# Kernel tuning notes

Measured on AMD Instinct MI355X. Metric: run time of the kernel, lower is better.

Reference implementation:

```python
import jax, jax.numpy as jnp
import numpy as np

N, E, G = 50000, 800000, 64
IN, HID, T, EDGE_DIM, HLS = 32, 64, 2, 2, 32
# deg histogram: all nodes degree 16 -> avg_deg['log'] = log(16+1)
AVG_LOG = float(np.log(17.0))


def _pna(x, src, dst, eattr, We, be, Wpre, bpre, Wpost, bpost, Wlin, blin):
    """PNAConv with aggregators [mean,min,max,std], scalers [identity,amp,att],
    towers=T, pre_layers=1, post_layers=1, divide_input=False."""
    n, F = x.shape
    enc = eattr @ We + be                                   # [E, F] edge encoder
    # message: concat(x_i, x_j, edge) -> per-tower Linear(3F -> F)
    h = jnp.concatenate([x[dst], x[src], enc], axis=-1)     # [E, 3F] (same for all towers)
    m = jnp.einsum('ef,tfo->eto', h, Wpre) + bpre           # [E, T, F]
    ones = jnp.ones((m.shape[0],), m.dtype)
    cnt = jax.ops.segment_sum(ones, dst, num_segments=n)    # in-degree [N]
    d = jnp.maximum(cnt, 1.0)[:, None, None]
    s = jax.ops.segment_sum(m, dst, num_segments=n)
    mean = s / d
    msq = jax.ops.segment_sum(m * m, dst, num_segments=n) / d
    std = jnp.sqrt(jax.nn.relu(msq - mean * mean) + 1e-5)
    has = (cnt > 0)[:, None, None]
    mn = jnp.where(has, jax.ops.segment_min(m, dst, num_segments=n), 0.0)
    mx = jnp.where(has, jax.ops.segment_max(m, dst, num_segments=n), 0.0)
    agg = jnp.concatenate([mean, mn, mx, std], axis=-1)     # [N, T, 4F]
    logd = jnp.log(d + 1.0)
    scaled = jnp.concatenate([agg, agg * (logd / AVG_LOG), agg * (AVG_LOG / logd)], axis=-1)  # [N,T,12F]
    xt = jnp.broadcast_to(x[:, None, :], (n, Wpre.shape[0], F))
    out = jnp.concatenate([xt, scaled], axis=-1)            # [N, T, 13F]
    o = jnp.einsum('nti,tio->nto', out, Wpost) + bpost      # [N, T, F_out]
    return o.reshape(n, -1) @ Wlin + blin                   # [N, HID]


def setup_inputs():
    key = jax.random.key(0)
    ks = iter(jax.random.split(key, 48))
    def p(shape):
        return jax.random.normal(next(ks), shape, jnp.float32) * 0.05
    inp = {}
    inp['x'] = jax.random.normal(next(ks), (N, IN), jnp.float32)
    inp['edge_attr'] = jax.random.normal(next(ks), (E, EDGE_DIM), jnp.float32)
    inp['hls_attr'] = jax.random.normal(next(ks), (G, HLS), jnp.float32)
    inp['edge_index'] = jax.random.randint(next(ks), (2, E), 0, N)
    inp['batch'] = jnp.sort(jax.random.randint(next(ks), (N,), 0, G))
    Fo = HID // T
    for l, Fin in enumerate([IN, HID]):
        inp[f'We{l}'] = p((EDGE_DIM, Fin)); inp[f'be{l}'] = jnp.zeros((Fin,), jnp.float32)
        inp[f'Wpre{l}'] = p((T, 3 * Fin, Fin)); inp[f'bpre{l}'] = jnp.zeros((T, Fin), jnp.float32)
        inp[f'Wpost{l}'] = p((T, 13 * Fin, Fo)); inp[f'bpost{l}'] = jnp.zeros((T, Fo), jnp.float32)
        inp[f'Wlin{l}'] = p((HID, HID)); inp[f'blin{l}'] = jnp.zeros((HID,), jnp.float32)
    inp['W1'] = p((HID + HLS, 64)); inp['b1'] = jnp.zeros((64,), jnp.float32)
    inp['W2'] = p((64, 64)); inp['b2'] = jnp.zeros((64,), jnp.float32)
    inp['W3'] = p((64, 1)); inp['b3'] = jnp.zeros((1,), jnp.float32)
    return inp


def reference(x, edge_attr, hls_attr,
              We0, be0, Wpre0, bpre0, Wpost0, bpost0, Wlin0, blin0,
              We1, be1, Wpre1, bpre1, Wpost1, bpost1, Wlin1, blin1,
              W1, b1, W2, b2, W3, b3,
              edge_index, batch):
    src, dst = edge_index[0], edge_index[1]
    h = jax.nn.relu(_pna(x, src, dst, edge_attr, We0, be0, Wpre0, bpre0, Wpost0, bpost0, Wlin0, blin0))
    h = jax.nn.relu(_pna(h, src, dst, edge_attr, We1, be1, Wpre1, bpre1, Wpost1, bpost1, Wlin1, blin1))
    g = jax.ops.segment_sum(h, batch, num_segments=G)       # global_add_pool [G, HID]
    g = jnp.concatenate([g, hls_attr], axis=-1)
    g = jax.nn.relu(g @ W1 + b1)
    g = jax.nn.relu(g @ W2 + b2)
    return g @ W3 + b3                                      # [G, 1]
```

## Files before the change

### kernel.cpp

```cpp
#include <hip/hip_runtime.h>
#include <math.h>
#include <float.h>

#define NN 50000
#define EE 800000
#define CAP 64

#define NB 196
#define SPAN 256
#define BCAP 4608

typedef unsigned short ushort_t;
typedef short short8 __attribute__((ext_vector_type(8)));
typedef float floatx4 __attribute__((ext_vector_type(4)));

__device__ __constant__ float kAVG_LOG = 2.8332133440562162f;

__device__ inline ushort_t f2bf(float v) {
    union { float f; unsigned u; } x; x.f = v;
    unsigned r = x.u + 0x7fffu + ((x.u >> 16) & 1u);
    return (ushort_t)(r >> 16);
}
__device__ inline float bf2f(ushort_t b) {
    union { unsigned u; float f; } x; x.u = ((unsigned)b) << 16; return x.f;
}
__device__ inline float bitsf(unsigned u) {
    union { unsigned u; float f; } x; x.u = u; return x.f;
}
__device__ inline void splitbf(float v, ushort_t& hi, ushort_t& lo) {
    hi = f2bf(v);
    lo = f2bf(v - bf2f(hi));
}

template <int F>
__device__ void prep_ab_dev(const float* __restrict__ We, const float* __restrict__ be,
                            const float* __restrict__ Wpre, const float* __restrict__ bpre,
                            float* __restrict__ U, float* __restrict__ Wab,
                            float* __restrict__ bias_ab) {
    const int TF = 2 * F;
    int tid = threadIdx.x;
    for (int idx = tid; idx < 2 * TF; idx += 256) {
        int c = idx / TF, f = idx % TF;
        int t = f / F, o = f % F;
        float s = 0.f;
        for (int g = 0; g < F; ++g)
            s += We[c * F + g] * Wpre[((size_t)t * 3 * F + 2 * F + g) * F + o];
        U[idx] = s;
    }
    for (int idx = tid; idx < F * 2 * TF; idx += 256) {
        int g = idx / (2 * TF), cc = idx % (2 * TF);
        int t, o, row;
        if (cc < TF) { t = cc / F; o = cc % F; row = g; }
        else { int c2 = cc - TF; t = c2 / F; o = c2 % F; row = F + g; }
        Wab[idx] = Wpre[((size_t)t * 3 * F + row) * F + o];
    }
    for (int cc = tid; cc < 2 * TF; cc += 256) {
        float v = 0.f;
        if (cc < TF) {
            int t = cc / F, o = cc % F;
            float s = 0.f;
            for (int g = 0; g < F; ++g)
                s += be[g] * Wpre[((size_t)t * 3 * F + 2 * F + g) * F + o];
            v = s + bpre[t * F + o];
        }
        bias_ab[cc] = v;
    }
}

template <int F>
__device__ void prep_zf_elem(int idx, const float* __restrict__ Wpost, const float* __restrict__ Wlin,
                             ushort_t* __restrict__ Bh, ushort_t* __restrict__ Bl) {
    const int KT = 9 * F;
    int jg = idx / KT, k = idx - jg * KT;
    int b = jg >> 6, j = jg & 63;
    float v = 0.f;
    if (k < F) {
        if (b == 0) {
#pragma unroll
            for (int t = 0; t < 2; ++t)
#pragma unroll
                for (int c = 0; c < 32; ++c)
                    v += Wpost[((size_t)t * 13 * F + k) * 32 + c] * Wlin[(t * 32 + c) * 64 + j];
        }
    } else {
        int r = k - F;
        int t = r / (4 * F), rr = r - t * 4 * F;
#pragma unroll
        for (int c = 0; c < 32; ++c)
            v += Wpost[((size_t)t * 13 * F + F + b * 4 * F + rr) * 32 + c] * Wlin[(t * 32 + c) * 64 + j];
    }
    ushort_t h_, l_;
    splitbf(v, h_, l_);
    Bh[(size_t)jg * KT + k] = h_;
    Bl[(size_t)jg * KT + k] = l_;
}

#define NZ0 216
#define NZ1 432
#define PREPB (NZ0 + NZ1 + 3)
#define INITB 6250

__global__ __launch_bounds__(256) void prep_init(
    const float* We0, const float* be0, const float* Wpre0, const float* bpre0,
    const float* Wpost0, const float* Wlin0, const float* bpost0, const float* blin0,
    const float* We1, const float* be1, const float* Wpre1, const float* bpre1,
    const float* Wpost1, const float* Wlin1, const float* bpost1, const float* blin1,
    float* U0, float* Wab0, float* bias_ab0, ushort_t* Bh0, ushort_t* Bl0, float* bias_zf0,
    float* U1, float* Wab1, float* bias_ab1, ushort_t* Bh1, ushort_t* Bl1, float* bias_zf1,
    int* gcount, float* pool, const float* __restrict__ x, ushort_t* __restrict__ xb) {
    int b = blockIdx.x;
    int tid = threadIdx.x;
    if (b >= PREPB) {
        int i = (b - PREPB) * 256 + tid;
        if (i < NN * 32) xb[i] = f2bf(x[i]);
        if (i < NB) gcount[i] = 0;
        if (i < 64 * 64) pool[i] = 0.f;
        return;
    }
    if (b < NZ0) {
        prep_zf_elem<32>(b * 256 + tid, Wpost0, Wlin0, Bh0, Bl0);
    } else if (b < NZ0 + NZ1) {
        prep_zf_elem<64>((b - NZ0) * 256 + tid, Wpost1, Wlin1, Bh1, Bl1);
    } else if (b == NZ0 + NZ1) {
        prep_ab_dev<32>(We0, be0, Wpre0, bpre0, U0, Wab0, bias_ab0);
    } else if (b == NZ0 + NZ1 + 1) {
        prep_ab_dev<64>(We1, be1, Wpre1, bpre1, U1, Wab1, bias_ab1);
    } else {
        for (int j = tid; j < 64; j += 256) {
            float s0 = blin0[j], s1 = blin1[j];
#pragma unroll
            for (int t = 0; t < 2; ++t)
#pragma unroll
                for (int c = 0; c < 32; ++c) {
                    s0 += bpost0[t * 32 + c] * Wlin0[(t * 32 + c) * 64 + j];
                    s1 += bpost1[t * 32 + c] * Wlin1[(t * 32 + c) * 64 + j];
                }
            bias_zf0[j] = s0;
            bias_zf1[j] = s1;
        }
    }
}

__global__ __launch_bounds__(1024) void partition_edges(
    const int* __restrict__ ei, const float* __restrict__ ea,
    int* __restrict__ gcount, uint2* __restrict__ part) {
    __shared__ int hist[NB];
    __shared__ int lbase[NB];
    int tid = threadIdx.x;
    int e0 = blockIdx.x * 4096;
    for (int i = tid; i < NB; i += 1024) hist[i] = 0;
    __syncthreads();
    int bq[4], rnk[4];
    unsigned px[4], py[4];
#pragma unroll
    for (int q = 0; q < 4; ++q) {
        int e = e0 + q * 1024 + tid;
        bq[q] = -1;
        if (e < EE) {
            int s = ei[e];
            int d = ei[EE + e];
            float2 v = *(const float2*)(ea + 2 * e);
            bq[q] = d >> 8;
            px[q] = ((unsigned)(d & 255) << 16) | (unsigned)s;
            py[q] = ((unsigned)f2bf(v.y) << 16) | (unsigned)f2bf(v.x);
            rnk[q] = atomicAdd(&hist[bq[q]], 1);
        }
    }
    __syncthreads();
    for (int i = tid; i < NB; i += 1024)
        lbase[i] = atomicAdd(&gcount[i], hist[i]);
    __syncthreads();
#pragma unroll
    for (int q = 0; q < 4; ++q) {
        if (bq[q] >= 0) {
            int slot = lbase[bq[q]] + rnk[q];
            if (slot < BCAP)
                part[(size_t)bq[q] * BCAP + slot] = make_uint2(px[q], py[q]);
        }
    }
}

__device__ void csr_fill_block(int g, const int* __restrict__ gcount,
                               const uint2* __restrict__ part,
                               int* __restrict__ cnt, uint2* __restrict__ csr) {
    __shared__ int lcnt[SPAN];
    int tid = threadIdx.x;
    lcnt[tid] = 0;
    __syncthreads();
    int total = gcount[g];
    if (total > BCAP) total = BCAP;
    size_t pbase = (size_t)g * BCAP;
    for (int i = tid; i < total; i += 256) {
        uint2 rec = part[pbase + i];
        int rel = rec.x >> 16;
        int src = rec.x & 0xffff;
        int p = atomicAdd(&lcnt[rel], 1);
        if (p < CAP) {
            int node = (g << 8) + rel;
            csr[(size_t)node * CAP + p] = make_uint2((unsigned)src, rec.y);
        }
    }
    __syncthreads();
    int node = (g << 8) + tid;
    if (node < NN) cnt[node] = lcnt[tid];
}

__device__ void gemm_bias_block(const float* __restrict__ A, const float* __restrict__ B,
                                const float* __restrict__ bias, float* __restrict__ Ca,
                                ushort_t* __restrict__ Cb, int M, int K, int Ncols, int bstart,
                                int mb, int cb) {
    __shared__ float As[32][132];
    __shared__ float Bs[32][68];
    int m0 = mb * 128, c0 = cb * 64;
    int tid = threadIdx.x;
    int tx = tid & 15, ty = tid >> 4;
    int ms = tid >> 3, u = tid & 7;
    float acc[8][4] = {};
    for (int k0 = 0; k0 < K; k0 += 32) {
#pragma unroll
        for (int p = 0; p < 4; ++p) {
            int m = ms + 32 * p;
            int gm = m0 + m;
            float4 v = make_float4(0.f, 0.f, 0.f, 0.f);
            if (gm < M) v = *(const float4*)(A + (size_t)gm * K + k0 + u * 4);
            As[u * 4 + 0][m] = v.x; As[u * 4 + 1][m] = v.y;
            As[u * 4 + 2][m] = v.z; As[u * 4 + 3][m] = v.w;
        }
#pragma unroll
        for (int p = 0; p < 2; ++p) {
            int idx = tid + 256 * p;
            int kk = idx >> 4, q = idx & 15;
            *(float4*)&Bs[kk][q * 4] = *(const float4*)(B + (size_t)(k0 + kk) * Ncols + c0 + q * 4);
        }
        __syncthreads();
#pragma unroll 8
        for (int k = 0; k < 32; ++k) {
            float a0[8], b0[4];
            *(float4*)&a0[0] = *(const float4*)&As[k][ty * 8];
            *(float4*)&a0[4] = *(const float4*)&As[k][ty * 8 + 4];
            *(float4*)&b0[0] = *(const float4*)&Bs[k][tx * 4];
#pragma unroll
            for (int i = 0; i < 8; ++i)
#pragma unroll
                for (int j = 0; j < 4; ++j) acc[i][j] = fmaf(a0[i], b0[j], acc[i][j]);
        }
        __syncthreads();
    }
    float bj[4];
#pragma unroll
    for (int j = 0; j < 4; ++j) bj[j] = bias[c0 + tx * 4 + j];
    bool bside = (c0 >= bstart);
    int TFw = bstart;
#pragma unroll
    for (int i = 0; i < 8; ++i) {
        int gm = m0 + ty * 8 + i;
        if (gm >= M) continue;
        float v0 = acc[i][0] + bj[0], v1 = acc[i][1] + bj[1];
        float v2 = acc[i][2] + bj[2], v3 = acc[i][3] + bj[3];
        if (!bside) {
            *(float4*)(Ca + (size_t)gm * TFw + c0 + tx * 4) = make_float4(v0, v1, v2, v3);
        } else {
            ushort4 w;
            w.x = f2bf(v0); w.y = f2bf(v1); w.z = f2bf(v2); w.w = f2bf(v3);
            *(ushort4*)(Cb + (size_t)gm * TFw + (c0 - bstart) + tx * 4) = w;
        }
    }
}

__global__ __launch_bounds__(256) void gemm_bias(const float* __restrict__ A, const float* __restrict__ B,
                                                 const float* __restrict__ bias, float* __restrict__ Ca,
                                                 ushort_t* __restrict__ Cb, int M, int K, int Ncols, int bstart) {
    gemm_bias_block(A, B, bias, Ca, Cb, M, K, Ncols, bstart, blockIdx.x, blockIdx.y);
}

__global__ __launch_bounds__(256) void csr_gemm0(
    const int* __restrict__ gcount, const uint2* __restrict__ part,
    int* __restrict__ cnt, uint2* __restrict__ csr,
    const float* __restrict__ A, const float* __restrict__ B, const float* __restrict__ bias,
    float* __restrict__ Ca, ushort_t* __restrict__ Cb) {
    int bx = blockIdx.x;
    if (bx % 5 == 0) {
        csr_fill_block(bx / 5, gcount, part, cnt, csr);
    } else {
        int idx = bx - 1 - bx / 5;
        gemm_bias_block(A, B, bias, Ca, Cb, NN, 32, 128, 64, idx % 391, idx / 391);
    }
}

template <int F>
__global__ __launch_bounds__(256) void aggregate(const float* __restrict__ ABa, const ushort_t* __restrict__ ABb,
                                                 const int* __restrict__ cnt, const uint2* __restrict__ csr,
                                                 const float* __restrict__ U,
                                                 ushort_t* __restrict__ agg_b, float2* __restrict__ sc) {
    const int TF = 2 * F;
    const int FPL = TF / 64;
    int lane = threadIdx.x & 63;
    int n = blockIdx.x * 4 + (threadIdx.x >> 6);
    if (n >= NN) return;
    n = __builtin_amdgcn_readfirstlane(n);
    int f0 = FPL * lane;

    float base[FPL], u0[FPL], u1[FPL], sum[FPL], sq[FPL], mn[FPL], mx[FPL];
#pragma unroll
    for (int r = 0; r < FPL; ++r) {
        base[r] = ABa[(size_t)n * TF + f0 + r];
        u0[r] = U[f0 + r];
        u1[r] = U[TF + f0 + r];
        sum[r] = 0.f; sq[r] = 0.f; mn[r] = FLT_MAX; mx[r] = -FLT_MAX;
    }
    int deg = cnt[n];
    int ec = deg < CAP ? deg : CAP;
    const uint2* __restrict__ p = csr + (size_t)n * CAP;

    int e = 0;
    for (; e + 8 <= ec; e += 8) {
        uint4 c0 = *(const uint4*)(p + e);
        uint4 c1 = *(const uint4*)(p + e + 2);
        uint4 c2 = *(const uint4*)(p + e + 4);
        uint4 c3 = *(const uint4*)(p + e + 6);
        unsigned sb[8] = {c0.x, c0.z, c1.x, c1.z, c2.x, c2.z, c3.x, c3.z};
        unsigned ep[8] = {c0.y, c0.w, c1.y, c1.w, c2.y, c2.w, c3.y, c3.w};
        unsigned wv[8];
#pragma unroll
        for (int i = 0; i < 8; ++i) {
            const ushort_t* row = ABb + (size_t)sb[i] * TF;
            if constexpr (FPL == 2)
                wv[i] = *(const unsigned*)(row + f0);
            else
                wv[i] = row[f0];
        }
#pragma unroll
        for (int i = 0; i < 8; ++i) {
            float ex = bitsf(ep[i] << 16);
            float ey = bitsf(ep[i] & 0xffff0000u);
            float v[FPL];
            if constexpr (FPL == 2) {
                v[0] = bitsf(wv[i] << 16);
                v[1] = bitsf(wv[i] & 0xffff0000u);
            } else {
                v[0] = bitsf(wv[i] << 16);
            }
#pragma unroll
            for (int r = 0; r < FPL; ++r) {
                float q = fmaf(ex, u0[r], fmaf(ey, u1[r], v[r]));
                sum[r] += q;
                sq[r] = fmaf(q, q, sq[r]);
                mn[r] = fminf(mn[r], q);
                mx[r] = fmaxf(mx[r], q);
            }
        }
    }
    for (; e < ec; ++e) {
        uint2 ent = p[e];
        const ushort_t* row = ABb + (size_t)ent.x * TF;
        unsigned wvt;
        if constexpr (FPL == 2) wvt = *(const unsigned*)(row + f0);
        else wvt = row[f0];
        float ex = bitsf(ent.y << 16);
        float ey = bitsf(ent.y & 0xffff0000u);
        float v[FPL];
        if constexpr (FPL == 2) {
            v[0] = bitsf(wvt << 16);
            v[1] = bitsf(wvt & 0xffff0000u);
        } else {
            v[0] = bitsf(wvt << 16);
        }
#pragma unroll
        for (int r = 0; r < FPL; ++r) {
            float q = fmaf(ex, u0[r], fmaf(ey, u1[r], v[r]));
            sum[r] += q;
            sq[r] = fmaf(q, q, sq[r]);
            mn[r] = fminf(mn[r], q);
            mx[r] = fmaxf(mx[r], q);
        }
    }

    float d = (float)(deg > 1 ? deg : 1);
    float inv_d = 1.f / d;
    bool has = deg > 0;
#pragma unroll
    for (int r = 0; r < FPL; ++r) {
        float mean_q = sum[r] * inv_d;
        float var = sq[r] * inv_d - mean_q * mean_q;
        float stdv = sqrtf(fmaxf(var, 0.f) + 1e-5f);
        float mean = has ? base[r] + mean_q : 0.f;
        float vmn = has ? base[r] + mn[r] : 0.f;
        float vmx = has ? base[r] + mx[r] : 0.f;
        int f = f0 + r;
        int t = f / F, o = f - t * F;
        size_t rowb = (size_t)n * (4 * TF) + (size_t)t * (4 * F);
        agg_b[rowb + o] = f2bf(mean);
        agg_b[rowb + F + o] = f2bf(vmn);
        agg_b[rowb + 2 * F + o] = f2bf(vmx);
        agg_b[rowb + 3 * F + o] = f2bf(stdv);
    }
    if (lane == 0) {
        float logd = logf(d + 1.f);
        sc[n] = make_float2(logd / kAVG_LOG, kAVG_LOG / logd);
    }
}

template <int F, bool POOL>
__global__ __launch_bounds__(256, 4) void gemm_zf(
    const ushort_t* __restrict__ xs_b, const ushort_t* __restrict__ agg_b,
    const ushort_t* __restrict__ Bh, const ushort_t* __restrict__ Bl,
    const float* __restrict__ bias_zf, const float2* __restrict__ sc,
    float* __restrict__ H, ushort_t* __restrict__ H_b,
    const int* __restrict__ batch, float* __restrict__ pool) {
    const int KT = 9 * F;
    extern __shared__ char smem[];
    ushort_t* A_s  = (ushort_t*)smem;
    ushort_t* Bh_s = A_s + 64 * 40;
    ushort_t* Bl_s = Bh_s + 192 * 40;
    float* hbuf = (float*)smem;

    int m0 = blockIdx.x * 64;
    int tid = threadIdx.x;
    int lane = tid & 63;
    int wave = tid >> 6;
    int ln = lane & 15, quad = lane >> 4;

    floatx4 acc[4][3];
#pragma unroll
    for (int i = 0; i < 4; ++i)
#pragma unroll
        for (int j = 0; j < 3; ++j) acc[i][j] = (floatx4)(0.f);

    int arow = tid >> 2, asg = tid & 3;
    int bcol[3], bsg[3];
#pragma unroll
    for (int p = 0; p < 3; ++p) {
        int idx = tid + 256 * p;
        bcol[p] = idx >> 2;
        bsg[p] = idx & 3;
    }

    const short8 zero8 = {0, 0, 0, 0, 0, 0, 0, 0};
    short8 pa, pbh[3], pbl[3];
    {
        int c0 = asg * 8;
        int gm = m0 + arow;
        pa = zero8;
        if (gm < NN) pa = *(const short8*)(xs_b + (size_t)gm * F + c0);
#pragma unroll
        for (int p = 0; p < 3; ++p) {
            pbh[p] = *(const short8*)(Bh + (size_t)bcol[p] * KT + bsg[p] * 8);
            pbl[p] = *(const short8*)(Bl + (size_t)bcol[p] * KT + bsg[p] * 8);
        }
    }

    for (int k0 = 0; k0 < KT; k0 += 32) {
        *(short8*)&A_s[arow * 40 + asg * 8] = pa;
#pragma unroll
        for (int p = 0; p < 3; ++p) {
            *(short8*)&Bh_s[bcol[p] * 40 + bsg[p] * 8] = pbh[p];
            *(short8*)&Bl_s[bcol[p] * 40 + bsg[p] * 8] = pbl[p];
        }
        __syncthreads();
        short8 bh[3], bl[3];
#pragma unroll
        for (int b = 0; b < 3; ++b) {
            int col = b * 64 + wave * 16 + ln;
            bh[b] = *(short8*)&Bh_s[col * 40 + quad * 8];
            bl[b] = *(short8*)&Bl_s[col * 40 + quad * 8];
        }
        int kn = k0 + 32;
        if (kn < KT) {
            int c0 = kn + asg * 8;
            int gm = m0 + arow;
            pa = zero8;
            if (gm < NN) {
                pa = (c0 < F) ? *(const short8*)(xs_b + (size_t)gm * F + c0)
                              : *(const short8*)(agg_b + (size_t)gm * 8 * F + (c0 - F));
            }
#pragma unroll
            for (int p = 0; p < 3; ++p) {
                pbh[p] = *(const short8*)(Bh + (size_t)bcol[p] * KT + kn + bsg[p] * 8);
                pbl[p] = *(const short8*)(Bl + (size_t)bcol[p] * KT + kn + bsg[p] * 8);
            }
        }
#pragma unroll
        for (int rf = 0; rf < 4; ++rf) {
            short8 ah = *(short8*)&A_s[(rf * 16 + ln) * 40 + quad * 8];
#pragma unroll
            for (int b = 0; b < 3; ++b) {
                acc[rf][b] = __builtin_amdgcn_mfma_f32_16x16x32_bf16(ah, bh[b], acc[rf][b], 0, 0, 0);
                acc[rf][b] = __builtin_amdgcn_mfma_f32_16x16x32_bf16(ah, bl[b], acc[rf][b], 0, 0, 0);
            }
        }
        __syncthreads();
    }

    int ocol = wave * 16 + ln;
    float bcolv = bias_zf[ocol];

#pragma unroll
    for (int rf = 0; rf < 4; ++rf) {
#pragma unroll
        for (int reg = 0; reg < 4; ++reg) {
            int r = rf * 16 + quad * 4 + reg;
            int gm = m0 + r;
            float2 s = make_float2(0.f, 0.f);
            if (gm < NN) s = sc[gm];
            float y = acc[rf][0][reg] + s.x * acc[rf][1][reg] + s.y * acc[rf][2][reg] + bcolv;
            y = fmaxf(y, 0.f);
            if (POOL) {
                hbuf[r * 68 + ocol] = (gm < NN) ? y : 0.f;
            } else if (gm < NN) {
                H[(size_t)gm * 64 + ocol] = y;
                H_b[(size_t)gm * 64 + ocol] = f2bf(y);
            }
        }
    }
    if (POOL) {
        __syncthreads();
        int col = tid & 63, grp = tid >> 6;
        float a = 0.f;
        int cur = -1;
        for (int i = 0; i < 16; ++i) {
            int r = grp * 16 + i;
            int gm = m0 + r;
            if (gm >= NN) break;
            int b = batch[gm];
            if (b != cur) {
                if (cur >= 0) atomicAdd(&pool[cur * 64 + col], a);
                cur = b; a = 0.f;
            }
            a += hbuf[r * 68 + col];
        }
        if (cur >= 0) atomicAdd(&pool[cur * 64 + col], a);
    }
}

__global__ __launch_bounds__(256) void head_kernel(const float* __restrict__ gpool, const float* __restrict__ hls,
                                                   const float* __restrict__ W1, const float* __restrict__ b1,
                                                   const float* __restrict__ W2, const float* __restrict__ b2,
                                                   const float* __restrict__ W3, const float* __restrict__ b3,
                                                   float* __restrict__ out) {
    __shared__ float gin[64][96];
    __shared__ float r1[64][64];
    __shared__ float r2[64][64];
    int tid = threadIdx.x;
    for (int idx = tid; idx < 64 * 96; idx += 256) {
        int g = idx / 96, j = idx % 96;
        gin[g][j] = (j < 64) ? gpool[g * 64 + j] : hls[g * 32 + (j - 64)];
    }
    __syncthreads();
    for (int idx = tid; idx < 64 * 64; idx += 256) {
        int g = idx / 64, j = idx % 64;
        float acc = b1[j];
        for (int k = 0; k < 96; ++k) acc = fmaf(gin[g][k], W1[k * 64 + j], acc);
        r1[g][j] = fmaxf(acc, 0.f);
    }
    __syncthreads();
    for (int idx = tid; idx < 64 * 64; idx += 256) {
        int g = idx / 64, j = idx % 64;
        float acc = b2[j];
        for (int k = 0; k < 64; ++k) acc = fmaf(r1[g][k], W2[k * 64 + j], acc);
        r2[g][j] = fmaxf(acc, 0.f);
    }
    __syncthreads();
    if (tid < 64) {
        float acc = b3[0];
        for (int k = 0; k < 64; ++k) acc = fmaf(r2[tid][k], W3[k], acc);
        out[tid] = acc;
    }
}

extern "C" void kernel_launch(void* const* d_in, const int* in_sizes, int n_in,
                              void* d_out, int out_size, void* d_ws, size_t ws_size,
                              hipStream_t stream) {
    (void)in_sizes; (void)n_in; (void)out_size; (void)ws_size;
    const float* x     = (const float*)d_in[0];
    const float* eattr = (const float*)d_in[1];
    const float* hls   = (const float*)d_in[2];
    const int*   eidx  = (const int*)d_in[3];
    const int*   batch = (const int*)d_in[4];
    const float* We[2]    = {(const float*)d_in[5],  (const float*)d_in[13]};
    const float* be[2]    = {(const float*)d_in[6],  (const float*)d_in[14]};
    const float* Wpre[2]  = {(const float*)d_in[7],  (const float*)d_in[15]};
    const float* bpre[2]  = {(const float*)d_in[8],  (const float*)d_in[16]};
    const float* Wpost[2] = {(const float*)d_in[9],  (const float*)d_in[17]};
    const float* bpost[2] = {(const float*)d_in[10], (const float*)d_in[18]};
    const float* Wlin[2]  = {(const float*)d_in[11], (const float*)d_in[19]};
    const float* blin[2]  = {(const float*)d_in[12], (const float*)d_in[20]};
    const float* W1 = (const float*)d_in[21]; const float* b1 = (const float*)d_in[22];
    const float* W2 = (const float*)d_in[23]; const float* b2 = (const float*)d_in[24];
    const float* W3 = (const float*)d_in[25]; const float* b3 = (const float*)d_in[26];
    float* out = (float*)d_out;

    char* ws = (char*)d_ws;
    size_t off = 0;
    auto carve = [&](size_t bytes) -> char* {
        char* p = ws + off;
        off = (off + bytes + 255) & ~(size_t)255;
        return p;
    };
    int*      cnt      = (int*)carve((size_t)NN * 4);
    uint2*    csr      = (uint2*)carve((size_t)NN * CAP * 8);
    float*    ABa      = (float*)carve((size_t)NN * 128 * 4);
    ushort_t* ABb      = (ushort_t*)carve((size_t)NN * 128 * 2);
    ushort_t* agg_b    = (ushort_t*)carve((size_t)NN * 512 * 2);
    float2*   sc       = (float2*)carve((size_t)NN * 8);
    ushort_t* xs_b     = (ushort_t*)carve((size_t)NN * 32 * 2);
    float*    h1       = (float*)carve((size_t)NN * 64 * 4);
    ushort_t* h1_b     = (ushort_t*)carve((size_t)NN * 64 * 2);
    float*    U0       = (float*)carve(256 * 4);
    float*    U1       = (float*)carve(256 * 4);
    float*    Wab0     = (float*)carve(16384 * 4);
    float*    Wab1     = (float*)carve(16384 * 4);
    float*    bias_ab0 = (float*)carve(256 * 4);
    float*    bias_ab1 = (float*)carve(256 * 4);
    ushort_t* Bh0      = (ushort_t*)carve((size_t)192 * 288 * 2);
    ushort_t* Bl0      = (ushort_t*)carve((size_t)192 * 288 * 2);
    ushort_t* Bh1      = (ushort_t*)carve((size_t)192 * 576 * 2);
    ushort_t* Bl1      = (ushort_t*)carve((size_t)192 * 576 * 2);
    float*    bias_zf0 = (float*)carve(64 * 4);
    float*    bias_zf1 = (float*)carve(64 * 4);
    float*    pool     = (float*)carve(64 * 64 * 4);
    int*      gcount   = (int*)carve(NB * 4);
    uint2*    part     = (uint2*)agg_b;

    const int MB128 = (NN + 127) / 128;
    const int MB64  = (NN + 63) / 64;
    const int SMEM_ZF = (64 * 40 + 192 * 40 + 192 * 40) * 2;
    const int FUSEDB = NB + MB128 * 2;

    prep_init<<<PREPB + INITB, 256, 0, stream>>>(
        We[0], be[0], Wpre[0], bpre[0], Wpost[0], Wlin[0], bpost[0], blin[0],
        We[1], be[1], Wpre[1], bpre[1], Wpost[1], Wlin[1], bpost[1], blin[1],
        U0, Wab0, bias_ab0, Bh0, Bl0, bias_zf0,
        U1, Wab1, bias_ab1, Bh1, Bl1, bias_zf1,
        gcount, pool, x, xs_b);

    partition_edges<<<(EE + 4095) / 4096, 1024, 0, stream>>>(eidx, eattr, gcount, part);

    csr_gemm0<<<FUSEDB, 256, 0, stream>>>(gcount, part, cnt, csr, x, Wab0, bias_ab0, ABa, ABb);
    aggregate<32><<<(NN + 3) / 4, 256, 0, stream>>>(ABa, ABb, cnt, csr, U0, agg_b, sc);
    gemm_zf<32, false><<<MB64, 256, SMEM_ZF, stream>>>(xs_b, agg_b, Bh0, Bl0, bias_zf0, sc,
                                                       h1, h1_b, batch, pool);

    gemm_bias<<<dim3(MB128, 4), 256, 0, stream>>>(h1, Wab1, bias_ab1, ABa, ABb, NN, 64, 256, 128);
    aggregate<64><<<(NN + 3) / 4, 256, 0, stream>>>(ABa, ABb, cnt, csr, U1, agg_b, sc);
    gemm_zf<64, true><<<MB64, 256, SMEM_ZF, stream>>>(h1_b, agg_b, Bh1, Bl1, bias_zf1, sc,
                                                      nullptr, nullptr, batch, pool);

    head_kernel<<<1, 256, 0, stream>>>(pool, hls, W1, b1, W2, b2, W3, b3, out);
}
```

Before: 349.9 us.

## Enlarge gemm_zf tile to 128 rows, load A directly, double-buffer B

The gemm_zf kernel now covers 128 rows per block instead of 64. Each wave loads its A fragments straight from global memory into registers, skipping the shared-memory A staging. The B tiles are double-buffered in shared memory, which drops one __syncthreads per k-step. This cuts barrier and LDS traffic and reuses each B tile across more rows, at the cost of more registers (8x3 accumulators plus 8 A fragments), occupancy lowered to 2 blocks per SIMD, and redundant A loads across the four waves.

```diff
diff --git a/kernel.cpp b/kernel.cpp
--- a/kernel.cpp
+++ b/kernel.cpp
@@ -401,32 +401,31 @@
 }
 
 template <int F, bool POOL>
-__global__ __launch_bounds__(256, 4) void gemm_zf(
+__global__ __launch_bounds__(256, 2) void gemm_zf(
     const ushort_t* __restrict__ xs_b, const ushort_t* __restrict__ agg_b,
     const ushort_t* __restrict__ Bh, const ushort_t* __restrict__ Bl,
     const float* __restrict__ bias_zf, const float2* __restrict__ sc,
     float* __restrict__ H, ushort_t* __restrict__ H_b,
     const int* __restrict__ batch, float* __restrict__ pool) {
     const int KT = 9 * F;
+    const int SEG = 192 * 40;
     extern __shared__ char smem[];
-    ushort_t* A_s  = (ushort_t*)smem;
-    ushort_t* Bh_s = A_s + 64 * 40;
-    ushort_t* Bl_s = Bh_s + 192 * 40;
+    ushort_t* Bh_s = (ushort_t*)smem;
+    ushort_t* Bl_s = Bh_s + 2 * SEG;
     float* hbuf = (float*)smem;
 
-    int m0 = blockIdx.x * 64;
+    int m0 = blockIdx.x * 128;
     int tid = threadIdx.x;
     int lane = tid & 63;
     int wave = tid >> 6;
     int ln = lane & 15, quad = lane >> 4;
 
-    floatx4 acc[4][3];
-#pragma unroll
-    for (int i = 0; i < 4; ++i)
+    floatx4 acc[8][3];
+#pragma unroll
+    for (int i = 0; i < 8; ++i)
 #pragma unroll
         for (int j = 0; j < 3; ++j) acc[i][j] = (floatx4)(0.f);
 
-    int arow = tid >> 2, asg = tid & 3;
     int bcol[3], bsg[3];
 #pragma unroll
     for (int p = 0; p < 3; ++p) {
@@ -436,43 +435,41 @@
     }
 
     const short8 zero8 = {0, 0, 0, 0, 0, 0, 0, 0};
-    short8 pa, pbh[3], pbl[3];
-    {
-        int c0 = asg * 8;
-        int gm = m0 + arow;
-        pa = zero8;
-        if (gm < NN) pa = *(const short8*)(xs_b + (size_t)gm * F + c0);
+    short8 pbh[3], pbl[3];
+#pragma unroll
+    for (int p = 0; p < 3; ++p) {
+        pbh[p] = *(const short8*)(Bh + (size_t)bcol[p] * KT + bsg[p] * 8);
+        pbl[p] = *(const short8*)(Bl + (size_t)bcol[p] * KT + bsg[p] * 8);
+    }
+
+    int cur = 0;
+    for (int k0 = 0; k0 < KT; k0 += 32) {
 #pragma unroll
         for (int p = 0; p < 3; ++p) {
-            pbh[p] = *(const short8*)(Bh + (size_t)bcol[p] * KT + bsg[p] * 8);
-            pbl[p] = *(const short8*)(Bl + (size_t)bcol[p] * KT + bsg[p] * 8);
-        }
-    }
-
-    for (int k0 = 0; k0 < KT; k0 += 32) {
-        *(short8*)&A_s[arow * 40 + asg * 8] = pa;
-#pragma unroll
-        for (int p = 0; p < 3; ++p) {
-            *(short8*)&Bh_s[bcol[p] * 40 + bsg[p] * 8] = pbh[p];
-            *(short8*)&Bl_s[bcol[p] * 40 + bsg[p] * 8] = pbl[p];
+            *(short8*)&Bh_s[cur * SEG + bcol[p] * 40 + bsg[p] * 8] = pbh[p];
+            *(short8*)&Bl_s[cur * SEG + bcol[p] * 40 + bsg[p] * 8] = pbl[p];
+        }
+        short8 ah[8];
+        int c0 = k0 + quad * 8;
+#pragma unroll
+        for (int rf = 0; rf < 8; ++rf) {
+            int gm = m0 + rf * 16 + ln;
+            ah[rf] = zero8;
+            if (gm < NN) {
+                ah[rf] = (c0 < F) ? *(const short8*)(xs_b + (size_t)gm * F + c0)
+                                  : *(const short8*)(agg_b + (size_t)gm * 8 * F + (c0 - F));
+            }
         }
         __syncthreads();
         short8 bh[3], bl[3];
 #pragma unroll
         for (int b = 0; b < 3; ++b) {
             int col = b * 64 + wave * 16 + ln;
-            bh[b] = *(short8*)&Bh_s[col * 40 + quad * 8];
-            bl[b] = *(short8*)&Bl_s[col * 40 + quad * 8];
+            bh[b] = *(short8*)&Bh_s[cur * SEG + col * 40 + quad * 8];
+            bl[b] = *(short8*)&Bl_s[cur * SEG + col * 40 + quad * 8];
         }
         int kn = k0 + 32;
         if (kn < KT) {
-            int c0 = kn + asg * 8;
-            int gm = m0 + arow;
-            pa = zero8;
-            if (gm < NN) {
-                pa = (c0 < F) ? *(const short8*)(xs_b + (size_t)gm * F + c0)
-                              : *(const short8*)(agg_b + (size_t)gm * 8 * F + (c0 - F));
-            }
 #pragma unroll
             for (int p = 0; p < 3; ++p) {
                 pbh[p] = *(const short8*)(Bh + (size_t)bcol[p] * KT + kn + bsg[p] * 8);
@@ -480,22 +477,23 @@
             }
         }
 #pragma unroll
-        for (int rf = 0; rf < 4; ++rf) {
-            short8 ah = *(short8*)&A_s[(rf * 16 + ln) * 40 + quad * 8];
+        for (int rf = 0; rf < 8; ++rf) {
 #pragma unroll
             for (int b = 0; b < 3; ++b) {
-                acc[rf][b] = __builtin_amdgcn_mfma_f32_16x16x32_bf16(ah, bh[b], acc[rf][b], 0, 0, 0);
-                acc[rf][b] = __builtin_amdgcn_mfma_f32_16x16x32_bf16(ah, bl[b], acc[rf][b], 0, 0, 0);
+                acc[rf][b] = __builtin_amdgcn_mfma_f32_16x16x32_bf16(ah[rf], bh[b], acc[rf][b], 0, 0, 0);
+                acc[rf][b] = __builtin_amdgcn_mfma_f32_16x16x32_bf16(ah[rf], bl[b], acc[rf][b], 0, 0, 0);
             }
         }
-        __syncthreads();
+        cur ^= 1;
     }
 
     int ocol = wave * 16 + ln;
     float bcolv = bias_zf[ocol];
 
-#pragma unroll
-    for (int rf = 0; rf < 4; ++rf) {
+    if (POOL) __syncthreads();
+
+#pragma unroll
+    for (int rf = 0; rf < 8; ++rf) {
 #pragma unroll
         for (int reg = 0; reg < 4; ++reg) {
             int r = rf * 16 + quad * 4 + reg;
@@ -516,19 +514,19 @@
         __syncthreads();
         int col = tid & 63, grp = tid >> 6;
         float a = 0.f;
-        int cur = -1;
-        for (int i = 0; i < 16; ++i) {
-            int r = grp * 16 + i;
+        int cur2 = -1;
+        for (int i = 0; i < 32; ++i) {
+            int r = grp * 32 + i;
             int gm = m0 + r;
             if (gm >= NN) break;
             int b = batch[gm];
-            if (b != cur) {
-                if (cur >= 0) atomicAdd(&pool[cur * 64 + col], a);
-                cur = b; a = 0.f;
+            if (b != cur2) {
+                if (cur2 >= 0) atomicAdd(&pool[cur2 * 64 + col], a);
+                cur2 = b; a = 0.f;
             }
             a += hbuf[r * 68 + col];
         }
-        if (cur >= 0) atomicAdd(&pool[cur * 64 + col], a);
+        if (cur2 >= 0) atomicAdd(&pool[cur2 * 64 + col], a);
     }
 }
 
@@ -622,8 +620,7 @@
     uint2*    part     = (uint2*)agg_b;
 
     const int MB128 = (NN + 127) / 128;
-    const int MB64  = (NN + 63) / 64;
-    const int SMEM_ZF = (64 * 40 + 192 * 40 + 192 * 40) * 2;
+    const int SMEM_ZF = 4 * 192 * 40 * 2;
     const int FUSEDB = NB + MB128 * 2;
 
     prep_init<<<PREPB + INITB, 256, 0, stream>>>(
@@ -637,13 +634,13 @@
 
     csr_gemm0<<<FUSEDB, 256, 0, stream>>>(gcount, part, cnt, csr, x, Wab0, bias_ab0, ABa, ABb);
     aggregate<32><<<(NN + 3) / 4, 256, 0, stream>>>(ABa, ABb, cnt, csr, U0, agg_b, sc);
-    gemm_zf<32, false><<<MB64, 256, SMEM_ZF, stream>>>(xs_b, agg_b, Bh0, Bl0, bias_zf0, sc,
-                                                       h1, h1_b, batch, pool);
+    gemm_zf<32, false><<<MB128, 256, SMEM_ZF, stream>>>(xs_b, agg_b, Bh0, Bl0, bias_zf0, sc,
+                                                        h1, h1_b, batch, pool);
 
     gemm_bias<<<dim3(MB128, 4), 256, 0, stream>>>(h1, Wab1, bias_ab1, ABa, ABb, NN, 64, 256, 128);
     aggregate<64><<<(NN + 3) / 4, 256, 0, stream>>>(ABa, ABb, cnt, csr, U1, agg_b, sc);
-    gemm_zf<64, true><<<MB64, 256, SMEM_ZF, stream>>>(h1_b, agg_b, Bh1, Bl1, bias_zf1, sc,
-                                                      nullptr, nullptr, batch, pool);
+    gemm_zf<64, true><<<MB128, 256, SMEM_ZF, stream>>>(h1_b, agg_b, Bh1, Bl1, bias_zf1, sc,
+                                                       nullptr, nullptr, batch, pool);
 
     head_kernel<<<1, 256, 0, stream>>>(pool, hls, W1, b1, W2, b2, W3, b3, out);
 }
```

Result: slower. 357.6 us (+2.2%).

## Load GEMM operands directly into MFMA fragment registers, dropping LDS staging

Applied to the files above, without the earlier changes.

The gemm_zf kernel no longer stages A and B tiles through shared memory with two barriers per k-step. Each wave now loads its MFMA operand fragments straight from global memory into registers, double-buffered, with the k-loop fully unrolled. Shared memory is allocated only for the pooling variant's epilogue buffer, and launch bounds drop to 3 blocks per SM to make room for the extra registers. The cost is redundant global/L2 reads, since every wave reloads all A rows and each B column is fetched by several lanes, plus higher register pressure.

```diff
diff --git a/kernel.cpp b/kernel.cpp
--- a/kernel.cpp
+++ b/kernel.cpp
@@ -401,7 +401,7 @@
 }
 
 template <int F, bool POOL>
-__global__ __launch_bounds__(256, 4) void gemm_zf(
+__global__ __launch_bounds__(256, 3) void gemm_zf(
     const ushort_t* __restrict__ xs_b, const ushort_t* __restrict__ agg_b,
     const ushort_t* __restrict__ Bh, const ushort_t* __restrict__ Bl,
     const float* __restrict__ bias_zf, const float2* __restrict__ sc,
@@ -409,9 +409,6 @@
     const int* __restrict__ batch, float* __restrict__ pool) {
     const int KT = 9 * F;
     extern __shared__ char smem[];
-    ushort_t* A_s  = (ushort_t*)smem;
-    ushort_t* Bh_s = A_s + 64 * 40;
-    ushort_t* Bl_s = Bh_s + 192 * 40;
     float* hbuf = (float*)smem;
 
     int m0 = blockIdx.x * 64;
@@ -426,69 +423,62 @@
 #pragma unroll
         for (int j = 0; j < 3; ++j) acc[i][j] = (floatx4)(0.f);
 
-    int arow = tid >> 2, asg = tid & 3;
-    int bcol[3], bsg[3];
-#pragma unroll
-    for (int p = 0; p < 3; ++p) {
-        int idx = tid + 256 * p;
-        bcol[p] = idx >> 2;
-        bsg[p] = idx & 3;
-    }
-
     const short8 zero8 = {0, 0, 0, 0, 0, 0, 0, 0};
-    short8 pa, pbh[3], pbl[3];
-    {
-        int c0 = asg * 8;
-        int gm = m0 + arow;
-        pa = zero8;
-        if (gm < NN) pa = *(const short8*)(xs_b + (size_t)gm * F + c0);
-#pragma unroll
-        for (int p = 0; p < 3; ++p) {
-            pbh[p] = *(const short8*)(Bh + (size_t)bcol[p] * KT + bsg[p] * 8);
-            pbl[p] = *(const short8*)(Bl + (size_t)bcol[p] * KT + bsg[p] * 8);
-        }
-    }
-
+
+    int grow[4];
+#pragma unroll
+    for (int rf = 0; rf < 4; ++rf) grow[rf] = m0 + rf * 16 + ln;
+    int gcol[3];
+#pragma unroll
+    for (int b = 0; b < 3; ++b) gcol[b] = b * 64 + wave * 16 + ln;
+
+    short8 a_cur[4], bh_cur[3], bl_cur[3];
+    short8 a_nxt[4], bh_nxt[3], bl_nxt[3];
+
+#pragma unroll
+    for (int rf = 0; rf < 4; ++rf) {
+        a_cur[rf] = zero8;
+        if (grow[rf] < NN) a_cur[rf] = *(const short8*)(xs_b + (size_t)grow[rf] * F + quad * 8);
+    }
+#pragma unroll
+    for (int b = 0; b < 3; ++b) {
+        bh_cur[b] = *(const short8*)(Bh + (size_t)gcol[b] * KT + quad * 8);
+        bl_cur[b] = *(const short8*)(Bl + (size_t)gcol[b] * KT + quad * 8);
+    }
+
+#pragma unroll
     for (int k0 = 0; k0 < KT; k0 += 32) {
-        *(short8*)&A_s[arow * 40 + asg * 8] = pa;
-#pragma unroll
-        for (int p = 0; p < 3; ++p) {
-            *(short8*)&Bh_s[bcol[p] * 40 + bsg[p] * 8] = pbh[p];
-            *(short8*)&Bl_s[bcol[p] * 40 + bsg[p] * 8] = pbl[p];
-        }
-        __syncthreads();
-        short8 bh[3], bl[3];
-#pragma unroll
-        for (int b = 0; b < 3; ++b) {
-            int col = b * 64 + wave * 16 + ln;
-            bh[b] = *(short8*)&Bh_s[col * 40 + quad * 8];
-            bl[b] = *(short8*)&Bl_s[col * 40 + quad * 8];
-        }
         int kn = k0 + 32;
         if (kn < KT) {
-            int c0 = kn + asg * 8;
-            int gm = m0 + arow;
-            pa = zero8;
-            if (gm < NN) {
-                pa = (c0 < F) ? *(const short8*)(xs_b + (size_t)gm * F + c0)
-                              : *(const short8*)(agg_b + (size_t)gm * 8 * F + (c0 - F));
+            int c0 = kn + quad * 8;
+#pragma unroll
+            for (int rf = 0; rf < 4; ++rf) {
+                a_nxt[rf] = zero8;
+                if (grow[rf] < NN) {
+                    a_nxt[rf] = (c0 < F) ? *(const short8*)(xs_b + (size_t)grow[rf] * F + c0)
+                                         : *(const short8*)(agg_b + (size_t)grow[rf] * 8 * F + (c0 - F));
+                }
             }
 #pragma unroll
-            for (int p = 0; p < 3; ++p) {
-                pbh[p] = *(const short8*)(Bh + (size_t)bcol[p] * KT + kn + bsg[p] * 8);
-                pbl[p] = *(const short8*)(Bl + (size_t)bcol[p] * KT + kn + bsg[p] * 8);
+            for (int b = 0; b < 3; ++b) {
+                bh_nxt[b] = *(const short8*)(Bh + (size_t)gcol[b] * KT + kn + quad * 8);
+                bl_nxt[b] = *(const short8*)(Bl + (size_t)gcol[b] * KT + kn + quad * 8);
             }
         }
 #pragma unroll
         for (int rf = 0; rf < 4; ++rf) {
-            short8 ah = *(short8*)&A_s[(rf * 16 + ln) * 40 + quad * 8];
 #pragma unroll
             for (int b = 0; b < 3; ++b) {
-                acc[rf][b] = __builtin_amdgcn_mfma_f32_16x16x32_bf16(ah, bh[b], acc[rf][b], 0, 0, 0);
-                acc[rf][b] = __builtin_amdgcn_mfma_f32_16x16x32_bf16(ah, bl[b], acc[rf][b], 0, 0, 0);
+                acc[rf][b] = __builtin_amdgcn_mfma_f32_16x16x32_bf16(a_cur[rf], bh_cur[b], acc[rf][b], 0, 0, 0);
+                acc[rf][b] = __builtin_amdgcn_mfma_f32_16x16x32_bf16(a_cur[rf], bl_cur[b], acc[rf][b], 0, 0, 0);
             }
         }
-        __syncthreads();
+        if (kn < KT) {
+#pragma unroll
+            for (int rf = 0; rf < 4; ++rf) a_cur[rf] = a_nxt[rf];
+#pragma unroll
+            for (int b = 0; b < 3; ++b) { bh_cur[b] = bh_nxt[b]; bl_cur[b] = bl_nxt[b]; }
+        }
     }
 
     int ocol = wave * 16 + ln;
@@ -623,7 +613,7 @@
 
     const int MB128 = (NN + 127) / 128;
     const int MB64  = (NN + 63) / 64;
-    const int SMEM_ZF = (64 * 40 + 192 * 40 + 192 * 40) * 2;
+    const int SMEM_POOL = 64 * 68 * 4;
     const int FUSEDB = NB + MB128 * 2;
 
     prep_init<<<PREPB + INITB, 256, 0, stream>>>(
@@ -637,13 +627,13 @@
 
     csr_gemm0<<<FUSEDB, 256, 0, stream>>>(gcount, part, cnt, csr, x, Wab0, bias_ab0, ABa, ABb);
     aggregate<32><<<(NN + 3) / 4, 256, 0, stream>>>(ABa, ABb, cnt, csr, U0, agg_b, sc);
-    gemm_zf<32, false><<<MB64, 256, SMEM_ZF, stream>>>(xs_b, agg_b, Bh0, Bl0, bias_zf0, sc,
-                                                       h1, h1_b, batch, pool);
+    gemm_zf<32, false><<<MB64, 256, 0, stream>>>(xs_b, agg_b, Bh0, Bl0, bias_zf0, sc,
+                                                 h1, h1_b, batch, pool);
 
     gemm_bias<<<dim3(MB128, 4), 256, 0, stream>>>(h1, Wab1, bias_ab1, ABa, ABb, NN, 64, 256, 128);
     aggregate<64><<<(NN + 3) / 4, 256, 0, stream>>>(ABa, ABb, cnt, csr, U1, agg_b, sc);
-    gemm_zf<64, true><<<MB64, 256, SMEM_ZF, stream>>>(h1_b, agg_b, Bh1, Bl1, bias_zf1, sc,
-                                                      nullptr, nullptr, batch, pool);
+    gemm_zf<64, true><<<MB64, 256, SMEM_POOL, stream>>>(h1_b, agg_b, Bh1, Bl1, bias_zf1, sc,
+                                                        nullptr, nullptr, batch, pool);
 
     head_kernel<<<1, 256, 0, stream>>>(pool, hls, W1, b1, W2, b2, W3, b3, out);
 }
```

New measurement: 397.0 us. 13.5% more time.

## Merge edge partition into prep kernel and widen gemm_zf to 128-row tiles

Applied to the files above, without the earlier changes.

Folds the edge-partition pass into the weight-prep/bf16-conversion kernel as extra blocks. That kernel now runs at 1024 threads, and the zeroing of gcount and pool moves to hipMemsetAsync so the partition blocks can atomically add into gcount in the same launch. gemm_zf now uses 512-thread blocks covering 128 rows, with 8 waves in a 2x4 arrangement, so each B tile staged in shared memory is reused across twice as many rows. The goal is fewer kernel launches and less B-tile reload traffic. The cost is larger shared memory per block, lower occupancy, and an extra sync before the pooling buffer reuses shared memory.

```diff
diff --git a/kernel.cpp b/kernel.cpp
--- a/kernel.cpp
+++ b/kernel.cpp
@@ -39,7 +39,7 @@
                             float* __restrict__ bias_ab) {
     const int TF = 2 * F;
     int tid = threadIdx.x;
-    for (int idx = tid; idx < 2 * TF; idx += 256) {
+    for (int idx = tid; idx < 2 * TF; idx += 1024) {
         int c = idx / TF, f = idx % TF;
         int t = f / F, o = f % F;
         float s = 0.f;
@@ -47,14 +47,14 @@
             s += We[c * F + g] * Wpre[((size_t)t * 3 * F + 2 * F + g) * F + o];
         U[idx] = s;
     }
-    for (int idx = tid; idx < F * 2 * TF; idx += 256) {
+    for (int idx = tid; idx < F * 2 * TF; idx += 1024) {
         int g = idx / (2 * TF), cc = idx % (2 * TF);
         int t, o, row;
         if (cc < TF) { t = cc / F; o = cc % F; row = g; }
         else { int c2 = cc - TF; t = c2 / F; o = c2 % F; row = F + g; }
         Wab[idx] = Wpre[((size_t)t * 3 * F + row) * F + o];
     }
-    for (int cc = tid; cc < 2 * TF; cc += 256) {
+    for (int cc = tid; cc < 2 * TF; cc += 1024) {
         float v = 0.f;
         if (cc < TF) {
             int t = cc / F, o = cc % F;
@@ -95,38 +95,70 @@
     Bl[(size_t)jg * KT + k] = l_;
 }
 
-#define NZ0 216
-#define NZ1 432
-#define PREPB (NZ0 + NZ1 + 3)
-#define INITB 6250
-
-__global__ __launch_bounds__(256) void prep_init(
+#define PARTB 196
+#define PZ0B  54
+#define PZ1B  108
+#define PINITB 1563
+
+__global__ __launch_bounds__(1024) void prep_part_init(
+    const int* __restrict__ ei, const float* __restrict__ ea,
+    int* __restrict__ gcount, uint2* __restrict__ part,
     const float* We0, const float* be0, const float* Wpre0, const float* bpre0,
     const float* Wpost0, const float* Wlin0, const float* bpost0, const float* blin0,
     const float* We1, const float* be1, const float* Wpre1, const float* bpre1,
     const float* Wpost1, const float* Wlin1, const float* bpost1, const float* blin1,
     float* U0, float* Wab0, float* bias_ab0, ushort_t* Bh0, ushort_t* Bl0, float* bias_zf0,
     float* U1, float* Wab1, float* bias_ab1, ushort_t* Bh1, ushort_t* Bl1, float* bias_zf1,
-    int* gcount, float* pool, const float* __restrict__ x, ushort_t* __restrict__ xb) {
+    const float* __restrict__ x, ushort_t* __restrict__ xb) {
+    __shared__ int hist[NB];
+    __shared__ int lbase[NB];
+    int tid = threadIdx.x;
     int b = blockIdx.x;
-    int tid = threadIdx.x;
-    if (b >= PREPB) {
-        int i = (b - PREPB) * 256 + tid;
-        if (i < NN * 32) xb[i] = f2bf(x[i]);
-        if (i < NB) gcount[i] = 0;
-        if (i < 64 * 64) pool[i] = 0.f;
+    if (b < PARTB) {
+        int e0 = b * 4096;
+        for (int i = tid; i < NB; i += 1024) hist[i] = 0;
+        __syncthreads();
+        int bq[4], rnk[4];
+        unsigned px[4], py[4];
+#pragma unroll
+        for (int q = 0; q < 4; ++q) {
+            int e = e0 + q * 1024 + tid;
+            bq[q] = -1;
+            if (e < EE) {
+                int s = ei[e];
+                int d = ei[EE + e];
+                float2 v = *(const float2*)(ea + 2 * e);
+                bq[q] = d >> 8;
+                px[q] = ((unsigned)(d & 255) << 16) | (unsigned)s;
+                py[q] = ((unsigned)f2bf(v.y) << 16) | (unsigned)f2bf(v.x);
+                rnk[q] = atomicAdd(&hist[bq[q]], 1);
+            }
+        }
+        __syncthreads();
+        for (int i = tid; i < NB; i += 1024)
+            lbase[i] = atomicAdd(&gcount[i], hist[i]);
+        __syncthreads();
+#pragma unroll
+        for (int q = 0; q < 4; ++q) {
+            if (bq[q] >= 0) {
+                int slot = lbase[bq[q]] + rnk[q];
+                if (slot < BCAP)
+                    part[(size_t)bq[q] * BCAP + slot] = make_uint2(px[q], py[q]);
+            }
+        }
         return;
     }
-    if (b < NZ0) {
-        prep_zf_elem<32>(b * 256 + tid, Wpost0, Wlin0, Bh0, Bl0);
-    } else if (b < NZ0 + NZ1) {
-        prep_zf_elem<64>((b - NZ0) * 256 + tid, Wpost1, Wlin1, Bh1, Bl1);
-    } else if (b == NZ0 + NZ1) {
+    b -= PARTB;
+    if (b < PZ0B) {
+        prep_zf_elem<32>(b * 1024 + tid, Wpost0, Wlin0, Bh0, Bl0);
+    } else if (b < PZ0B + PZ1B) {
+        prep_zf_elem<64>((b - PZ0B) * 1024 + tid, Wpost1, Wlin1, Bh1, Bl1);
+    } else if (b == PZ0B + PZ1B) {
         prep_ab_dev<32>(We0, be0, Wpre0, bpre0, U0, Wab0, bias_ab0);
-    } else if (b == NZ0 + NZ1 + 1) {
+    } else if (b == PZ0B + PZ1B + 1) {
         prep_ab_dev<64>(We1, be1, Wpre1, bpre1, U1, Wab1, bias_ab1);
-    } else {
-        for (int j = tid; j < 64; j += 256) {
+    } else if (b == PZ0B + PZ1B + 2) {
+        for (int j = tid; j < 64; j += 1024) {
             float s0 = blin0[j], s1 = blin1[j];
 #pragma unroll
             for (int t = 0; t < 2; ++t)
@@ -138,45 +170,9 @@
             bias_zf0[j] = s0;
             bias_zf1[j] = s1;
         }
-    }
-}
-
-__global__ __launch_bounds__(1024) void partition_edges(
-    const int* __restrict__ ei, const float* __restrict__ ea,
-    int* __restrict__ gcount, uint2* __restrict__ part) {
-    __shared__ int hist[NB];
-    __shared__ int lbase[NB];
-    int tid = threadIdx.x;
-    int e0 = blockIdx.x * 4096;
-    for (int i = tid; i < NB; i += 1024) hist[i] = 0;
-    __syncthreads();
-    int bq[4], rnk[4];
-    unsigned px[4], py[4];
-#pragma unroll
-    for (int q = 0; q < 4; ++q) {
-        int e = e0 + q * 1024 + tid;
-        bq[q] = -1;
-        if (e < EE) {
-            int s = ei[e];
-            int d = ei[EE + e];
-            float2 v = *(const float2*)(ea + 2 * e);
-            bq[q] = d >> 8;
-            px[q] = ((unsigned)(d & 255) << 16) | (unsigned)s;
-            py[q] = ((unsigned)f2bf(v.y) << 16) | (unsigned)f2bf(v.x);
-            rnk[q] = atomicAdd(&hist[bq[q]], 1);
-        }
-    }
-    __syncthreads();
-    for (int i = tid; i < NB; i += 1024)
-        lbase[i] = atomicAdd(&gcount[i], hist[i]);
-    __syncthreads();
-#pragma unroll
-    for (int q = 0; q < 4; ++q) {
-        if (bq[q] >= 0) {
-            int slot = lbase[bq[q]] + rnk[q];
-            if (slot < BCAP)
-                part[(size_t)bq[q] * BCAP + slot] = make_uint2(px[q], py[q]);
-        }
+    } else {
+        int i = (b - (PZ0B + PZ1B + 3)) * 1024 + tid;
+        if (i < NN * 32) xb[i] = f2bf(x[i]);
     }
 }
 
@@ -401,7 +397,7 @@
 }
 
 template <int F, bool POOL>
-__global__ __launch_bounds__(256, 4) void gemm_zf(
+__global__ __launch_bounds__(512, 2) void gemm_zf(
     const ushort_t* __restrict__ xs_b, const ushort_t* __restrict__ agg_b,
     const ushort_t* __restrict__ Bh, const ushort_t* __restrict__ Bl,
     const float* __restrict__ bias_zf, const float2* __restrict__ sc,
@@ -410,14 +406,16 @@
     const int KT = 9 * F;
     extern __shared__ char smem[];
     ushort_t* A_s  = (ushort_t*)smem;
-    ushort_t* Bh_s = A_s + 64 * 40;
+    ushort_t* Bh_s = A_s + 128 * 40;
     ushort_t* Bl_s = Bh_s + 192 * 40;
     float* hbuf = (float*)smem;
 
-    int m0 = blockIdx.x * 64;
+    int m0 = blockIdx.x * 128;
     int tid = threadIdx.x;
     int lane = tid & 63;
     int wave = tid >> 6;
+    int wr = wave >> 2;
+    int wc = wave & 3;
     int ln = lane & 15, quad = lane >> 4;
 
     floatx4 acc[4][3];
@@ -427,40 +425,47 @@
         for (int j = 0; j < 3; ++j) acc[i][j] = (floatx4)(0.f);
 
     int arow = tid >> 2, asg = tid & 3;
-    int bcol[3], bsg[3];
-#pragma unroll
-    for (int p = 0; p < 3; ++p) {
-        int idx = tid + 256 * p;
+    int bcol[2], bsg[2];
+    bool bok[2];
+#pragma unroll
+    for (int p = 0; p < 2; ++p) {
+        int idx = tid + 512 * p;
+        bok[p] = idx < 768;
         bcol[p] = idx >> 2;
         bsg[p] = idx & 3;
     }
 
     const short8 zero8 = {0, 0, 0, 0, 0, 0, 0, 0};
-    short8 pa, pbh[3], pbl[3];
+    short8 pa, pbh[2], pbl[2];
     {
         int c0 = asg * 8;
         int gm = m0 + arow;
         pa = zero8;
         if (gm < NN) pa = *(const short8*)(xs_b + (size_t)gm * F + c0);
 #pragma unroll
-        for (int p = 0; p < 3; ++p) {
-            pbh[p] = *(const short8*)(Bh + (size_t)bcol[p] * KT + bsg[p] * 8);
-            pbl[p] = *(const short8*)(Bl + (size_t)bcol[p] * KT + bsg[p] * 8);
+        for (int p = 0; p < 2; ++p) {
+            pbh[p] = zero8; pbl[p] = zero8;
+            if (bok[p]) {
+                pbh[p] = *(const short8*)(Bh + (size_t)bcol[p] * KT + bsg[p] * 8);
+                pbl[p] = *(const short8*)(Bl + (size_t)bcol[p] * KT + bsg[p] * 8);
+            }
         }
     }
 
     for (int k0 = 0; k0 < KT; k0 += 32) {
         *(short8*)&A_s[arow * 40 + asg * 8] = pa;
 #pragma unroll
-        for (int p = 0; p < 3; ++p) {
-            *(short8*)&Bh_s[bcol[p] * 40 + bsg[p] * 8] = pbh[p];
-            *(short8*)&Bl_s[bcol[p] * 40 + bsg[p] * 8] = pbl[p];
+        for (int p = 0; p < 2; ++p) {
+            if (bok[p]) {
+                *(short8*)&Bh_s[bcol[p] * 40 + bsg[p] * 8] = pbh[p];
+                *(short8*)&Bl_s[bcol[p] * 40 + bsg[p] * 8] = pbl[p];
+            }
         }
         __syncthreads();
         short8 bh[3], bl[3];
 #pragma unroll
         for (int b = 0; b < 3; ++b) {
-            int col = b * 64 + wave * 16 + ln;
+            int col = b * 64 + wc * 16 + ln;
             bh[b] = *(short8*)&Bh_s[col * 40 + quad * 8];
             bl[b] = *(short8*)&Bl_s[col * 40 + quad * 8];
         }
@@ -474,14 +479,16 @@
                               : *(const short8*)(agg_b + (size_t)gm * 8 * F + (c0 - F));
             }
 #pragma unroll
-            for (int p = 0; p < 3; ++p) {
-                pbh[p] = *(const short8*)(Bh + (size_t)bcol[p] * KT + kn + bsg[p] * 8);
-                pbl[p] = *(const short8*)(Bl + (size_t)bcol[p] * KT + kn + bsg[p] * 8);
+            for (int p = 0; p < 2; ++p) {
+                if (bok[p]) {
+                    pbh[p] = *(const short8*)(Bh + (size_t)bcol[p] * KT + kn + bsg[p] * 8);
+                    pbl[p] = *(const short8*)(Bl + (size_t)bcol[p] * KT + kn + bsg[p] * 8);
+                }
             }
         }
 #pragma unroll
         for (int rf = 0; rf < 4; ++rf) {
-            short8 ah = *(short8*)&A_s[(rf * 16 + ln) * 40 + quad * 8];
+            short8 ah = *(short8*)&A_s[((wr * 4 + rf) * 16 + ln) * 40 + quad * 8];
 #pragma unroll
             for (int b = 0; b < 3; ++b) {
                 acc[rf][b] = __builtin_amdgcn_mfma_f32_16x16x32_bf16(ah, bh[b], acc[rf][b], 0, 0, 0);
@@ -491,14 +498,16 @@
         __syncthreads();
     }
 
-    int ocol = wave * 16 + ln;
+    int ocol = wc * 16 + ln;
     float bcolv = bias_zf[ocol];
 
+    if (POOL) __syncthreads();
+
 #pragma unroll
     for (int rf = 0; rf < 4; ++rf) {
 #pragma unroll
         for (int reg = 0; reg < 4; ++reg) {
-            int r = rf * 16 + quad * 4 + reg;
+            int r = (wr * 4 + rf) * 16 + quad * 4 + reg;
             int gm = m0 + r;
             float2 s = make_float2(0.f, 0.f);
             if (gm < NN) s = sc[gm];
@@ -622,28 +631,30 @@
     uint2*    part     = (uint2*)agg_b;
 
     const int MB128 = (NN + 127) / 128;
-    const int MB64  = (NN + 63) / 64;
-    const int SMEM_ZF = (64 * 40 + 192 * 40 + 192 * 40) * 2;
+    const int SMEM_ZF = (128 * 40 + 192 * 40 + 192 * 40) * 2;
     const int FUSEDB = NB + MB128 * 2;
-
-    prep_init<<<PREPB + INITB, 256, 0, stream>>>(
+    const int MERGEDB = PARTB + PZ0B + PZ1B + 3 + PINITB;
+
+    hipMemsetAsync(gcount, 0, NB * 4, stream);
+    hipMemsetAsync(pool, 0, 64 * 64 * 4, stream);
+
+    prep_part_init<<<MERGEDB, 1024, 0, stream>>>(
+        eidx, eattr, gcount, part,
         We[0], be[0], Wpre[0], bpre[0], Wpost[0], Wlin[0], bpost[0], blin[0],
         We[1], be[1], Wpre[1], bpre[1], Wpost[1], Wlin[1], bpost[1], blin[1],
         U0, Wab0, bias_ab0, Bh0, Bl0, bias_zf0,
         U1, Wab1, bias_ab1, Bh1, Bl1, bias_zf1,
-        gcount, pool, x, xs_b);
-
-    partition_edges<<<(EE + 4095) / 4096, 1024, 0, stream>>>(eidx, eattr, gcount, part);
+        x, xs_b);
 
     csr_gemm0<<<FUSEDB, 256, 0, stream>>>(gcount, part, cnt, csr, x, Wab0, bias_ab0, ABa, ABb);
     aggregate<32><<<(NN + 3) / 4, 256, 0, stream>>>(ABa, ABb, cnt, csr, U0, agg_b, sc);
-    gemm_zf<32, false><<<MB64, 256, SMEM_ZF, stream>>>(xs_b, agg_b, Bh0, Bl0, bias_zf0, sc,
-                                                       h1, h1_b, batch, pool);
+    gemm_zf<32, false><<<MB128, 512, SMEM_ZF, stream>>>(xs_b, agg_b, Bh0, Bl0, bias_zf0, sc,
+                                                        h1, h1_b, batch, pool);
 
     gemm_bias<<<dim3(MB128, 4), 256, 0, stream>>>(h1, Wab1, bias_ab1, ABa, ABb, NN, 64, 256, 128);
     aggregate<64><<<(NN + 3) / 4, 256, 0, stream>>>(ABa, ABb, cnt, csr, U1, agg_b, sc);
-    gemm_zf<64, true><<<MB64, 256, SMEM_ZF, stream>>>(h1_b, agg_b, Bh1, Bl1, bias_zf1, sc,
-                                                      nullptr, nullptr, batch, pool);
+    gemm_zf<64, true><<<MB128, 512, SMEM_ZF, stream>>>(h1_b, agg_b, Bh1, Bl1, bias_zf1, sc,
+                                                       nullptr, nullptr, batch, pool);
 
     head_kernel<<<1, 256, 0, stream>>>(pool, hls, W1, b1, W2, b2, W3, b3, out);
 }
```

Measured after the change: 316.1 us. 1.11x faster.
